# Optimization experiments

Measured on AMD Instinct MI355X. Metric: run time of the kernel, lower is better.

## Reference

```python
import jax, jax.numpy as jnp
import numpy as np
from jax import lax

V = 50000      # VOCAB_SIZE
E = 256        # EMBEDDING_DIM
F = 128        # NUM_FILTERS = E/2 (feeds LSTM input_size)
K = 3          # KERNEL_SIZE
POOL = 2       # POOLING_SIZE (stride 1)
H = 128        # LSTM_HIDDEN_UNITS = E/2
NP = 128       # number of paths
L = 512        # tokens per path


def setup_inputs() -> dict:
    key = jax.random.key(0)
    ks = jax.random.split(key, 18)
    s = 0.05
    n = lambda k, shp: jax.random.normal(k, shp, dtype=jnp.float32) * s
    return {
        "path_data": jax.random.randint(ks[0], (NP, L), 0, V, dtype=jnp.int32),
        "query": 123,
        "emb_A": n(ks[1], (V, E)),          # SentEncoder embedding
        "emb_B": n(ks[2], (V, E)),          # query embedding
        "conv_w": n(ks[3], (F, E, K)),
        "conv_b": n(ks[4], (F,)),
        "w_ih_f": n(ks[5], (4 * H, F)),
        "w_hh_f": n(ks[6], (4 * H, H)),
        "b_ih_f": n(ks[7], (4 * H,)),
        "b_hh_f": n(ks[8], (4 * H,)),
        "w_ih_b": n(ks[9], (4 * H, F)),
        "w_hh_b": n(ks[10], (4 * H, H)),
        "b_ih_b": n(ks[11], (4 * H,)),
        "b_hh_b": n(ks[12], (4 * H,)),
        "d1_w": n(ks[13], (E, 2 * E)),
        "d1_b": n(ks[14], (E,)),
        "d2_w": n(ks[15], (1, E)),
        "d2_b": n(ks[16], (1,)),
    }


def _run_lstm(seq, w_ih, w_hh, b_ih, b_hh):
    # seq: [T, F] -> final hidden [H]; torch gate order i, f, g, o
    gx = seq @ w_ih.T + (b_ih + b_hh)  # [T, 4H] precomputed input gates

    def step(carry, g):
        h, c = carry
        g = g + h @ w_hh.T
        i, f, gg, o = jnp.split(g, 4)
        c = jax.nn.sigmoid(f) * c + jax.nn.sigmoid(i) * jnp.tanh(gg)
        h = jax.nn.sigmoid(o) * jnp.tanh(c)
        return (h, c), None

    z = jnp.zeros((H,), seq.dtype)
    (h, _), _ = lax.scan(step, (z, z), gx)
    return h


def reference(path_data, query, emb_A, emb_B, conv_w, conv_b,
              w_ih_f, w_hh_f, b_ih_f, b_hh_f,
              w_ih_b, w_hh_b, b_ih_b, b_hh_b,
              d1_w, d1_b, d2_w, d2_b):
    # --- SentEncoder, batched over paths ---
    x = emb_A[path_data]                  # [P, L, E]
    x = jnp.transpose(x, (0, 2, 1))       # [P, E, L]
    x = lax.conv_general_dilated(x, conv_w, (1,), 'VALID',
                                 dimension_numbers=('NCH', 'OIH', 'NCH'))
    x = jax.nn.relu(x + conv_b[None, :, None])         # [P, F, L-K+1]
    x = lax.reduce_window(x, -jnp.inf, lax.max, (1, 1, POOL), (1, 1, 1), 'VALID')
    x = jnp.transpose(x, (0, 2, 1))       # [P, T, F]

    def encode(seq):
        hf = _run_lstm(seq, w_ih_f, w_hh_f, b_ih_f, b_hh_f)
        hb = _run_lstm(seq[::-1], w_ih_b, w_hh_b, b_ih_b, b_hh_b)
        return jnp.concatenate([hf, hb])  # [2H] == [E]

    context = jax.vmap(encode)(x)         # [P, E]

    # --- 2-step additive attention pooling ---
    u = emb_B[query]                      # [E]
    for _ in range(2):
        u_rep = jnp.broadcast_to(u, (context.shape[0], E))
        cat = jnp.concatenate([context, u_rep], axis=1)        # [P, 2E]
        t = jnp.tanh(cat @ d1_w.T + d1_b)                      # [P, E]
        score = (t @ d2_w.T + d2_b).reshape(-1)                # [P]
        alpha = jax.nn.softmax(score)
        o = jnp.sum(alpha[:, None] * context, axis=0)          # [E]
        u = jnp.concatenate([u, o]) @ d1_w.T + d1_b            # [E]

    u = jax.nn.relu(u)
    pred = jax.nn.sigmoid(u @ d2_w.T + d2_b)
    return pred.squeeze()
```

## Files before the change

kernel.cpp:

```cpp
#include <hip/hip_runtime.h>
#include <hip/hip_bf16.h>

#define VOCAB 50000
#define EDIM 256
#define NF 128
#define KS 3
#define HID 128
#define NPATH 128
#define LSEQ 512
#define TCONV 510
#define TPOOL 509
#define CH 48

typedef unsigned int uint32;

__device__ __forceinline__ uint32 bf16r(float f) {
  uint32 u = __float_as_uint(f);
  return (u + 0x7fffu + ((u >> 16) & 1u)) >> 16;
}
__device__ __forceinline__ uint32 pack2(float a, float b) {
  return bf16r(a) | (bf16r(b) << 16);
}
__device__ __forceinline__ float blo(uint32 w) { return __uint_as_float(w << 16); }
__device__ __forceinline__ float bhi(uint32 w) { return __uint_as_float(w & 0xffff0000u); }

__device__ __forceinline__ float sigf(float x) { return 1.f / (1.f + __expf(-x)); }
__device__ __forceinline__ float tanhf_(float x) {
  float e = __expf(2.f * x);
  return (e - 1.f) / (e + 1.f);
}

__global__ void init_kernel(const float* __restrict__ conv_w,
                            const float* __restrict__ embB,
                            const int* __restrict__ query,
                            float* __restrict__ w_t, float* __restrict__ u_buf) {
  int idx = blockIdx.x * 256 + threadIdx.x;
  if (idx < EDIM * KS * NF) {
    int ek = idx >> 7, f = idx & (NF - 1);
    w_t[idx] = conv_w[f * (EDIM * KS) + ek];
  } else if (idx < EDIM * KS * NF + EDIM) {
    int i = idx - EDIM * KS * NF;
    u_buf[i] = embB[(size_t)query[0] * EDIM + i];
  }
}

__global__ __launch_bounds__(256) void conv_kernel(
    const int* __restrict__ path, const float* __restrict__ embA,
    const float* __restrict__ w_t, const float* __restrict__ conv_b,
    float* __restrict__ pooled) {
  __shared__ float xs[35 * EDIM];
  int t0 = blockIdx.x * 32;
  int p = blockIdx.y;
  const int* prow = path + p * LSEQ;
  for (int tok = 0; tok < 35; ++tok) {
    int tt = t0 + tok;
    float v = 0.f;
    if (tt < LSEQ) v = embA[(size_t)prow[tt] * EDIM + threadIdx.x];
    xs[tok * EDIM + threadIdx.x] = v;
  }
  __syncthreads();
  int f = threadIdx.x & (NF - 1), th = threadIdx.x >> 7;
  float b = conv_b[f];
  float acc[17];
#pragma unroll
  for (int i = 0; i < 17; ++i) acc[i] = b;
  for (int e = 0; e < EDIM; ++e) {
    float xv[19];
#pragma unroll
    for (int j = 0; j < 19; ++j) xv[j] = xs[(th * 16 + j) * EDIM + e];
#pragma unroll
    for (int k = 0; k < KS; ++k) {
      float wv = w_t[(e * KS + k) * NF + f];
#pragma unroll
      for (int i = 0; i < 17; ++i) acc[i] += wv * xv[i + k];
    }
  }
#pragma unroll
  for (int i = 0; i < 16; ++i) {
    int t = t0 + th * 16 + i;
    if (t < TPOOL) {
      float v = fmaxf(fmaxf(acc[i], 0.f), fmaxf(acc[i + 1], 0.f));
      pooled[((size_t)p * TPOOL + t) * NF + f] = v;
    }
  }
}

__global__ __launch_bounds__(512, 1) void lstm_kernel(
    const float* __restrict__ pooled,
    const float* __restrict__ w_ih_f, const float* __restrict__ w_hh_f,
    const float* __restrict__ b_ih_f, const float* __restrict__ b_hh_f,
    const float* __restrict__ w_ih_b, const float* __restrict__ w_hh_b,
    const float* __restrict__ b_ih_b, const float* __restrict__ b_hh_b,
    float* __restrict__ context) {
  __shared__ __align__(16) float x_l[CH][NF];
  __shared__ __align__(16) float gx_l[CH][4 * HID];
  __shared__ __align__(16) float h_l[HID];
  __shared__ float g_l[4 * HID];
  int p = blockIdx.x >> 1, d = blockIdx.x & 1;
  const float* w_ih = d ? w_ih_b : w_ih_f;
  const float* w_hh = d ? w_hh_b : w_hh_f;
  const float* b_ih = d ? b_ih_b : b_ih_f;
  const float* b_hh = d ? b_hh_b : b_hh_f;
  int tid = threadIdx.x;
  int gq = tid & 127, jq = tid >> 7;

  uint32 whh[64];
#pragma unroll
  for (int grp = 0; grp < 4; ++grp) {
#pragma unroll
    for (int q = 0; q < 8; ++q) {
      int jj = grp * 8 + q;
      float4 a = *(const float4*)(w_hh + (size_t)tid * HID + 4 * jj);
      whh[2 * jj] = pack2(a.x, a.y);
      whh[2 * jj + 1] = pack2(a.z, a.w);
    }
    __builtin_amdgcn_sched_barrier(0);
  }
  float bias4[4];
#pragma unroll
  for (int gi = 0; gi < 4; ++gi)
    bias4[gi] = b_ih[4 * gq + gi] + b_hh[4 * gq + gi];

  float c = 0.f, h = 0.f;
  if (tid < HID) h_l[tid] = 0.f;
  const float* prow = pooled + (size_t)p * TPOOL * NF;

  for (int t0 = 0; t0 < TPOOL; t0 += CH) {
    int ns = (TPOOL - t0 < CH) ? (TPOOL - t0) : CH;
    for (int q = tid; q < ns * (NF / 4); q += 512) {
      int j = q >> 5, e4 = q & 31;
      int ti = d ? (TPOOL - 1 - (t0 + j)) : (t0 + j);
      *(float4*)&x_l[j][e4 * 4] = *(const float4*)(prow + ti * NF + e4 * 4);
    }
    __syncthreads();
    const float* wbase = w_ih + (size_t)(4 * gq) * HID;
    for (int ps = 0; ps < 3; ++ps) {
      int jb = jq * 12 + ps * 4;
      float acc[4][4];
#pragma unroll
      for (int ji = 0; ji < 4; ++ji)
#pragma unroll
        for (int gi = 0; gi < 4; ++gi) acc[ji][gi] = bias4[gi];
      for (int jj = 0; jj < 32; ++jj) {
        float4 w0 = *(const float4*)(wbase + 0 * HID + 4 * jj);
        float4 w1 = *(const float4*)(wbase + 1 * HID + 4 * jj);
        float4 w2 = *(const float4*)(wbase + 2 * HID + 4 * jj);
        float4 w3 = *(const float4*)(wbase + 3 * HID + 4 * jj);
#pragma unroll
        for (int ji = 0; ji < 4; ++ji) {
          float4 xv = *(const float4*)&x_l[jb + ji][4 * jj];
          acc[ji][0] += w0.x * xv.x + w0.y * xv.y + w0.z * xv.z + w0.w * xv.w;
          acc[ji][1] += w1.x * xv.x + w1.y * xv.y + w1.z * xv.z + w1.w * xv.w;
          acc[ji][2] += w2.x * xv.x + w2.y * xv.y + w2.z * xv.z + w2.w * xv.w;
          acc[ji][3] += w3.x * xv.x + w3.y * xv.y + w3.z * xv.z + w3.w * xv.w;
        }
      }
#pragma unroll
      for (int ji = 0; ji < 4; ++ji)
        if (jb + ji < ns)
          *(float4*)&gx_l[jb + ji][4 * gq] =
              make_float4(acc[ji][0], acc[ji][1], acc[ji][2], acc[ji][3]);
    }
    __syncthreads();
    for (int j = 0; j < ns; ++j) {
      float a0 = gx_l[j][tid], a1 = 0.f, a2 = 0.f, a3 = 0.f;
      const float4* h4 = (const float4*)h_l;
#pragma unroll
      for (int jj = 0; jj < 32; ++jj) {
        float4 hv = h4[jj];
        uint32 wa = whh[2 * jj], wb = whh[2 * jj + 1];
        a0 += blo(wa) * hv.x;
        a1 += bhi(wa) * hv.y;
        a2 += blo(wb) * hv.z;
        a3 += bhi(wb) * hv.w;
      }
      g_l[tid] = (a0 + a1) + (a2 + a3);
      __syncthreads();
      if (tid < HID) {
        float gi = g_l[tid], gf = g_l[HID + tid], gg = g_l[2 * HID + tid],
              go = g_l[3 * HID + tid];
        c = sigf(gf) * c + sigf(gi) * tanhf_(gg);
        h = sigf(go) * tanhf_(c);
        h_l[tid] = h;
      }
      __syncthreads();
    }
  }
  if (tid < HID) context[p * 2 * HID + d * HID + tid] = h;
}

__global__ __launch_bounds__(256) void score_kernel(
    const float* __restrict__ context, const float* __restrict__ u_buf,
    const float* __restrict__ d1_w, const float* __restrict__ d1_b,
    const float* __restrict__ d2_w, const float* __restrict__ d2_b,
    float* __restrict__ scores) {
  __shared__ __align__(16) float cat[2 * EDIM];
  __shared__ float red[4];
  int p = blockIdx.x;
  int i = threadIdx.x;
  cat[i] = context[p * 2 * HID + i];
  cat[EDIM + i] = u_buf[i];
  __syncthreads();
  float acc = d1_b[i];
  const float4* wrow = (const float4*)(d1_w + (size_t)i * 2 * EDIM);
#pragma unroll 8
  for (int j = 0; j < 128; ++j) {
    float4 w4 = wrow[j];
    float4 c4 = *(const float4*)(&cat[4 * j]);
    acc += w4.x * c4.x + w4.y * c4.y + w4.z * c4.z + w4.w * c4.w;
  }
  float v = tanhf_(acc) * d2_w[i];
#pragma unroll
  for (int o = 32; o; o >>= 1) v += __shfl_down(v, o, 64);
  int lane = i & 63, w = i >> 6;
  if (lane == 0) red[w] = v;
  __syncthreads();
  if (i == 0) scores[p] = red[0] + red[1] + red[2] + red[3] + d2_b[0];
}

__global__ __launch_bounds__(256) void reduce_kernel(
    const float* __restrict__ context, const float* __restrict__ d1_w,
    const float* __restrict__ d1_b, const float* __restrict__ d2_w,
    const float* __restrict__ d2_b, const float* __restrict__ scores,
    float* __restrict__ u_buf, float* __restrict__ out, int final_step) {
  __shared__ float al[NPATH];
  __shared__ __align__(16) float uo[2 * EDIM];
  __shared__ float red[4];
  int i = threadIdx.x;
  int lane = i & 63, w = i >> 6;

  float s = (i < NPATH) ? scores[i] : -1e30f;
  float m = s;
#pragma unroll
  for (int o = 32; o; o >>= 1) m = fmaxf(m, __shfl_down(m, o, 64));
  if (lane == 0) red[w] = m;
  __syncthreads();
  m = fmaxf(fmaxf(red[0], red[1]), fmaxf(red[2], red[3]));
  __syncthreads();
  float e = (i < NPATH) ? __expf(s - m) : 0.f;
  float t = e;
#pragma unroll
  for (int o = 32; o; o >>= 1) t += __shfl_down(t, o, 64);
  if (lane == 0) red[w] = t;
  __syncthreads();
  float sum = red[0] + red[1] + red[2] + red[3];
  if (i < NPATH) al[i] = e / sum;
  __syncthreads();

  float o_i = 0.f;
  for (int p = 0; p < NPATH; ++p) o_i += al[p] * context[p * 2 * HID + i];
  uo[i] = u_buf[i];
  uo[EDIM + i] = o_i;
  __syncthreads();

  float un = d1_b[i];
  const float4* wrow = (const float4*)(d1_w + (size_t)i * 2 * EDIM);
#pragma unroll 8
  for (int j = 0; j < 128; ++j) {
    float4 w4 = wrow[j];
    float4 c4 = *(const float4*)(&uo[4 * j]);
    un += w4.x * c4.x + w4.y * c4.y + w4.z * c4.z + w4.w * c4.w;
  }
  if (!final_step) {
    u_buf[i] = un;
  } else {
    float v = fmaxf(un, 0.f) * d2_w[i];
#pragma unroll
    for (int o = 32; o; o >>= 1) v += __shfl_down(v, o, 64);
    if (lane == 0) red[w] = v;
    __syncthreads();
    if (i == 0) {
      float tot = red[0] + red[1] + red[2] + red[3] + d2_b[0];
      out[0] = 1.f / (1.f + __expf(-tot));
    }
  }
}

extern "C" void kernel_launch(void* const* d_in, const int* in_sizes, int n_in,
                              void* d_out, int out_size, void* d_ws, size_t ws_size,
                              hipStream_t stream) {
  const int* path = (const int*)d_in[0];
  const int* query = (const int*)d_in[1];
  const float* embA = (const float*)d_in[2];
  const float* embB = (const float*)d_in[3];
  const float* conv_w = (const float*)d_in[4];
  const float* conv_b = (const float*)d_in[5];
  const float* w_ih_f = (const float*)d_in[6];
  const float* w_hh_f = (const float*)d_in[7];
  const float* b_ih_f = (const float*)d_in[8];
  const float* b_hh_f = (const float*)d_in[9];
  const float* w_ih_b = (const float*)d_in[10];
  const float* w_hh_b = (const float*)d_in[11];
  const float* b_ih_b = (const float*)d_in[12];
  const float* b_hh_b = (const float*)d_in[13];
  const float* d1_w = (const float*)d_in[14];
  const float* d1_b = (const float*)d_in[15];
  const float* d2_w = (const float*)d_in[16];
  const float* d2_b = (const float*)d_in[17];
  float* out = (float*)d_out;

  float* ws = (float*)d_ws;
  float* pooled = ws;
  float* w_t = pooled + (size_t)NPATH * TPOOL * NF;
  float* context = w_t + EDIM * KS * NF;
  float* scores = context + NPATH * 2 * HID;
  float* u_buf = scores + NPATH;

  init_kernel<<<(EDIM * KS * NF + EDIM + 255) / 256, 256, 0, stream>>>(
      conv_w, embB, query, w_t, u_buf);
  conv_kernel<<<dim3(16, NPATH), 256, 0, stream>>>(path, embA, w_t, conv_b,
                                                   pooled);
  lstm_kernel<<<256, 512, 0, stream>>>(pooled, w_ih_f, w_hh_f, b_ih_f, b_hh_f,
                                       w_ih_b, w_hh_b, b_ih_b, b_hh_b, context);
  score_kernel<<<NPATH, 256, 0, stream>>>(context, u_buf, d1_w, d1_b, d2_w,
                                          d2_b, scores);
  reduce_kernel<<<1, 256, 0, stream>>>(context, d1_w, d1_b, d2_w, d2_b, scores,
                                       u_buf, out, 0);
  score_kernel<<<NPATH, 256, 0, stream>>>(context, u_buf, d1_w, d1_b, d2_w,
                                          d2_b, scores);
  reduce_kernel<<<1, 256, 0, stream>>>(context, d1_w, d1_b, d2_w, d2_b, scores,
                                       u_buf, out, 1);
}
```

Before: 2.036 ms.

## Switch LSTM matvecs to packed fp16 dot2 with pre-packed weights

Adds a pack kernel that converts the LSTM input and recurrent weights to packed fp16 pairs once per call. The input-gate projection and the recurrent matvec then use the fdot2 instruction on packed fp16 weights, inputs and hidden state, which halves LDS and global traffic and the instruction count per step. The hidden state is packed into fp16 pairs in shared memory with a lane shuffle. The trade-off is lower precision for x, h and the weights (fp16 instead of fp32/bf16), plus one extra small kernel launch.

```diff
diff --git a/kernel.cpp b/kernel.cpp
--- a/kernel.cpp
+++ b/kernel.cpp
@@ -13,16 +13,23 @@
 #define CH 48
 
 typedef unsigned int uint32;
-
-__device__ __forceinline__ uint32 bf16r(float f) {
-  uint32 u = __float_as_uint(f);
-  return (u + 0x7fffu + ((u >> 16) & 1u)) >> 16;
-}
-__device__ __forceinline__ uint32 pack2(float a, float b) {
-  return bf16r(a) | (bf16r(b) << 16);
-}
-__device__ __forceinline__ float blo(uint32 w) { return __uint_as_float(w << 16); }
-__device__ __forceinline__ float bhi(uint32 w) { return __uint_as_float(w & 0xffff0000u); }
+typedef _Float16 h2 __attribute__((ext_vector_type(2)));
+
+__device__ __forceinline__ float dot2(uint32 w, uint32 x, float acc) {
+#if defined(__has_builtin) && __has_builtin(__builtin_amdgcn_fdot2)
+  return __builtin_amdgcn_fdot2(__builtin_bit_cast(h2, w),
+                                __builtin_bit_cast(h2, x), acc, false);
+#else
+  h2 a = __builtin_bit_cast(h2, w), b = __builtin_bit_cast(h2, x);
+  return acc + (float)a[0] * (float)b[0] + (float)a[1] * (float)b[1];
+#endif
+}
+__device__ __forceinline__ uint32 packf16(float a, float b) {
+  h2 v;
+  v[0] = (_Float16)a;
+  v[1] = (_Float16)b;
+  return __builtin_bit_cast(uint32, v);
+}
 
 __device__ __forceinline__ float sigf(float x) { return 1.f / (1.f + __expf(-x)); }
 __device__ __forceinline__ float tanhf_(float x) {
@@ -42,6 +49,17 @@
     int i = idx - EDIM * KS * NF;
     u_buf[i] = embB[(size_t)query[0] * EDIM + i];
   }
+}
+
+__global__ __launch_bounds__(256) void pack_kernel(
+    const float* __restrict__ w_ih_f, const float* __restrict__ w_hh_f,
+    const float* __restrict__ w_ih_b, const float* __restrict__ w_hh_b,
+    uint32* __restrict__ wpack) {
+  int idx = blockIdx.x * 256 + threadIdx.x;
+  int m = idx >> 15;
+  int off = idx & 32767;
+  const float* src = m == 0 ? w_ih_f : m == 1 ? w_hh_f : m == 2 ? w_ih_b : w_hh_b;
+  wpack[idx] = packf16(src[2 * off], src[2 * off + 1]);
 }
 
 __global__ __launch_bounds__(256) void conv_kernel(
@@ -86,19 +104,17 @@
 }
 
 __global__ __launch_bounds__(512, 1) void lstm_kernel(
-    const float* __restrict__ pooled,
-    const float* __restrict__ w_ih_f, const float* __restrict__ w_hh_f,
+    const float* __restrict__ pooled, const uint32* __restrict__ wpack,
     const float* __restrict__ b_ih_f, const float* __restrict__ b_hh_f,
-    const float* __restrict__ w_ih_b, const float* __restrict__ w_hh_b,
     const float* __restrict__ b_ih_b, const float* __restrict__ b_hh_b,
     float* __restrict__ context) {
-  __shared__ __align__(16) float x_l[CH][NF];
+  __shared__ __align__(16) uint32 x_l[CH][NF / 2];
   __shared__ __align__(16) float gx_l[CH][4 * HID];
-  __shared__ __align__(16) float h_l[HID];
+  __shared__ __align__(16) uint32 h_p[HID / 2];
   __shared__ float g_l[4 * HID];
   int p = blockIdx.x >> 1, d = blockIdx.x & 1;
-  const float* w_ih = d ? w_ih_b : w_ih_f;
-  const float* w_hh = d ? w_hh_b : w_hh_f;
+  const uint32* wihp = wpack + (d ? 2 : 0) * 32768;
+  const uint32* whhp = wpack + (d ? 3 : 1) * 32768;
   const float* b_ih = d ? b_ih_b : b_ih_f;
   const float* b_hh = d ? b_hh_b : b_hh_f;
   int tid = threadIdx.x;
@@ -108,11 +124,13 @@
 #pragma unroll
   for (int grp = 0; grp < 4; ++grp) {
 #pragma unroll
-    for (int q = 0; q < 8; ++q) {
-      int jj = grp * 8 + q;
-      float4 a = *(const float4*)(w_hh + (size_t)tid * HID + 4 * jj);
-      whh[2 * jj] = pack2(a.x, a.y);
-      whh[2 * jj + 1] = pack2(a.z, a.w);
+    for (int q = 0; q < 4; ++q) {
+      int jj = grp * 4 + q;
+      uint4 t = *(const uint4*)(whhp + (size_t)tid * 64 + 4 * jj);
+      whh[4 * jj] = t.x;
+      whh[4 * jj + 1] = t.y;
+      whh[4 * jj + 2] = t.z;
+      whh[4 * jj + 3] = t.w;
     }
     __builtin_amdgcn_sched_barrier(0);
   }
@@ -122,18 +140,23 @@
     bias4[gi] = b_ih[4 * gq + gi] + b_hh[4 * gq + gi];
 
   float c = 0.f, h = 0.f;
-  if (tid < HID) h_l[tid] = 0.f;
+  if (tid < HID / 2) h_p[tid] = 0u;
   const float* prow = pooled + (size_t)p * TPOOL * NF;
 
   for (int t0 = 0; t0 < TPOOL; t0 += CH) {
     int ns = (TPOOL - t0 < CH) ? (TPOOL - t0) : CH;
-    for (int q = tid; q < ns * (NF / 4); q += 512) {
-      int j = q >> 5, e4 = q & 31;
+    for (int q = tid; q < ns * 16; q += 512) {
+      int j = q >> 4, b = q & 15;
       int ti = d ? (TPOOL - 1 - (t0 + j)) : (t0 + j);
-      *(float4*)&x_l[j][e4 * 4] = *(const float4*)(prow + ti * NF + e4 * 4);
+      const float* s = prow + ti * NF + b * 8;
+      float4 u = *(const float4*)s, v = *(const float4*)(s + 4);
+      x_l[j][4 * b] = packf16(u.x, u.y);
+      x_l[j][4 * b + 1] = packf16(u.z, u.w);
+      x_l[j][4 * b + 2] = packf16(v.x, v.y);
+      x_l[j][4 * b + 3] = packf16(v.z, v.w);
     }
     __syncthreads();
-    const float* wbase = w_ih + (size_t)(4 * gq) * HID;
+    const uint32* wbase = wihp + (size_t)(4 * gq) * 64;
     for (int ps = 0; ps < 3; ++ps) {
       int jb = jq * 12 + ps * 4;
       float acc[4][4];
@@ -141,18 +164,18 @@
       for (int ji = 0; ji < 4; ++ji)
 #pragma unroll
         for (int gi = 0; gi < 4; ++gi) acc[ji][gi] = bias4[gi];
-      for (int jj = 0; jj < 32; ++jj) {
-        float4 w0 = *(const float4*)(wbase + 0 * HID + 4 * jj);
-        float4 w1 = *(const float4*)(wbase + 1 * HID + 4 * jj);
-        float4 w2 = *(const float4*)(wbase + 2 * HID + 4 * jj);
-        float4 w3 = *(const float4*)(wbase + 3 * HID + 4 * jj);
+      for (int jj = 0; jj < 16; ++jj) {
+        uint4 w0 = *(const uint4*)(wbase + 0 * 64 + 4 * jj);
+        uint4 w1 = *(const uint4*)(wbase + 1 * 64 + 4 * jj);
+        uint4 w2 = *(const uint4*)(wbase + 2 * 64 + 4 * jj);
+        uint4 w3 = *(const uint4*)(wbase + 3 * 64 + 4 * jj);
 #pragma unroll
         for (int ji = 0; ji < 4; ++ji) {
-          float4 xv = *(const float4*)&x_l[jb + ji][4 * jj];
-          acc[ji][0] += w0.x * xv.x + w0.y * xv.y + w0.z * xv.z + w0.w * xv.w;
-          acc[ji][1] += w1.x * xv.x + w1.y * xv.y + w1.z * xv.z + w1.w * xv.w;
-          acc[ji][2] += w2.x * xv.x + w2.y * xv.y + w2.z * xv.z + w2.w * xv.w;
-          acc[ji][3] += w3.x * xv.x + w3.y * xv.y + w3.z * xv.z + w3.w * xv.w;
+          uint4 xv = *(const uint4*)&x_l[jb + ji][4 * jj];
+          acc[ji][0] = dot2(w0.w, xv.w, dot2(w0.z, xv.z, dot2(w0.y, xv.y, dot2(w0.x, xv.x, acc[ji][0]))));
+          acc[ji][1] = dot2(w1.w, xv.w, dot2(w1.z, xv.z, dot2(w1.y, xv.y, dot2(w1.x, xv.x, acc[ji][1]))));
+          acc[ji][2] = dot2(w2.w, xv.w, dot2(w2.z, xv.z, dot2(w2.y, xv.y, dot2(w2.x, xv.x, acc[ji][2]))));
+          acc[ji][3] = dot2(w3.w, xv.w, dot2(w3.z, xv.z, dot2(w3.y, xv.y, dot2(w3.x, xv.x, acc[ji][3]))));
         }
       }
 #pragma unroll
@@ -164,15 +187,13 @@
     __syncthreads();
     for (int j = 0; j < ns; ++j) {
       float a0 = gx_l[j][tid], a1 = 0.f, a2 = 0.f, a3 = 0.f;
-      const float4* h4 = (const float4*)h_l;
-#pragma unroll
-      for (int jj = 0; jj < 32; ++jj) {
-        float4 hv = h4[jj];
-        uint32 wa = whh[2 * jj], wb = whh[2 * jj + 1];
-        a0 += blo(wa) * hv.x;
-        a1 += bhi(wa) * hv.y;
-        a2 += blo(wb) * hv.z;
-        a3 += bhi(wb) * hv.w;
+#pragma unroll
+      for (int jj = 0; jj < 16; ++jj) {
+        uint4 hv = *(const uint4*)&h_p[4 * jj];
+        a0 = dot2(whh[4 * jj], hv.x, a0);
+        a1 = dot2(whh[4 * jj + 1], hv.y, a1);
+        a2 = dot2(whh[4 * jj + 2], hv.z, a2);
+        a3 = dot2(whh[4 * jj + 3], hv.w, a3);
       }
       g_l[tid] = (a0 + a1) + (a2 + a3);
       __syncthreads();
@@ -181,7 +202,8 @@
               go = g_l[3 * HID + tid];
         c = sigf(gf) * c + sigf(gi) * tanhf_(gg);
         h = sigf(go) * tanhf_(c);
-        h_l[tid] = h;
+        float hn = __shfl_down(h, 1, 64);
+        if (!(tid & 1)) h_p[tid >> 1] = packf16(h, hn);
       }
       __syncthreads();
     }
@@ -305,13 +327,15 @@
   float* context = w_t + EDIM * KS * NF;
   float* scores = context + NPATH * 2 * HID;
   float* u_buf = scores + NPATH;
+  uint32* wpack = (uint32*)(u_buf + EDIM);
 
   init_kernel<<<(EDIM * KS * NF + EDIM + 255) / 256, 256, 0, stream>>>(
       conv_w, embB, query, w_t, u_buf);
+  pack_kernel<<<512, 256, 0, stream>>>(w_ih_f, w_hh_f, w_ih_b, w_hh_b, wpack);
   conv_kernel<<<dim3(16, NPATH), 256, 0, stream>>>(path, embA, w_t, conv_b,
                                                    pooled);
-  lstm_kernel<<<256, 512, 0, stream>>>(pooled, w_ih_f, w_hh_f, b_ih_f, b_hh_f,
-                                       w_ih_b, w_hh_b, b_ih_b, b_hh_b, context);
+  lstm_kernel<<<256, 512, 0, stream>>>(pooled, wpack, b_ih_f, b_hh_f, b_ih_b,
+                                       b_hh_b, context);
   score_kernel<<<NPATH, 256, 0, stream>>>(context, u_buf, d1_w, d1_b, d2_w,
                                           d2_b, scores);
   reduce_kernel<<<1, 256, 0, stream>>>(context, d1_w, d1_b, d2_w, d2_b, scores,
```

Result: slower. 5.757 ms (+182.7%).
